# Performance work log

Hardware: AMD Instinct MI355X
Metric: run time of the kernel (lower is better)

The kernel has to match this reference:

```python
import jax, jax.numpy as jnp
import numpy as np

N_FFT = 64
HOP = 32
PAD = N_FFT // 2

def _window():
    # torch.hann_window(n_fft) is periodic: 0.5*(1 - cos(2*pi*n/N))
    n = jnp.arange(N_FFT, dtype=jnp.float32)
    return 0.5 * (1.0 - jnp.cos(2.0 * jnp.pi * n / N_FFT))

def _frame_idx(n_frames):
    return jnp.arange(n_frames)[:, None] * HOP + jnp.arange(N_FFT)[None, :]

def _stft(x):
    # x: [..., T] -> complex spectrogram [..., n_frames, F] (torch center=True, reflect pad)
    xp = jnp.pad(x, [(0, 0)] * (x.ndim - 1) + [(PAD, PAD)], mode='reflect')
    Tp = xp.shape[-1]
    n_frames = (Tp - N_FFT) // HOP + 1
    frames = xp[..., _frame_idx(n_frames)] * _window()  # [..., n_frames, n_fft]
    return jnp.fft.rfft(frames, axis=-1)

def _istft(spec, T):
    # spec: [..., n_frames, F] -> signal [..., T] (torch istft with length=T)
    w = _window()
    frames = jnp.fft.irfft(spec, n=N_FFT, axis=-1) * w  # [..., n_frames, n_fft]
    n_frames = frames.shape[-2]
    Tp = T + 2 * PAD
    idx = _frame_idx(n_frames)
    ola = jnp.zeros(frames.shape[:-2] + (Tp,), frames.dtype).at[..., idx].add(frames)
    env = jnp.zeros((Tp,), frames.dtype).at[idx].add(w * w)
    env = jnp.where(env > 1e-11, env, 1.0)
    return (ola / env)[..., PAD:PAD + T]

def reference(x, weight):
    # x: [B, C_in, T], weight: [C_out, C_in, F]
    B, C, T = x.shape
    U = _stft(x)  # [B, C_in, n_frames, F] complex
    # Linearity: sum over input channels in frequency domain, then one ISTFT per output channel.
    Yr = jnp.einsum('oif,binf->bonf', weight, U.real)
    Yi = jnp.einsum('oif,binf->bonf', weight, U.imag)
    Y = Yr + 1j * Yi  # [B, C_out, n_frames, F]
    return _istft(Y, T)  # [B, C_out, T]

def setup_inputs() -> dict:
    key = jax.random.key(0)
    k1, k2 = jax.random.split(key)
    B, C_in, C_out, T = 8, 64, 64, 16384
    x = jax.random.normal(k1, (B, C_in, T), dtype=jnp.float32)
    weight = jax.random.normal(k2, (C_out, C_in, N_FFT // 2 + 1), dtype=jnp.float32)
    return {"x": x, "weight": weight}
```

## Files before the change

kernel.cpp:

```cpp
#include <hip/hip_runtime.h>
#include <cstddef>

#define TT 16384
#define NFRAMES 513
#define NFP 520
#define BNP (8 * NFP)
#define PI32 0.09817477042468103870f

typedef unsigned int u32;
typedef unsigned short u16;
typedef __attribute__((ext_vector_type(8))) short bf16x8;
typedef __attribute__((ext_vector_type(4))) float f32x4;

#define TAB_WBF 0
#define TAB_BM  (33 * 64 * 72)
#define TAB_BTA (TAB_BM + 80 * 72)
#define TAB_TOT (TAB_BTA + 64 * 72)
#define TF_EINV 0

__device__ __forceinline__ float b2f(u16 h) {
  union { u32 u; float f; } v; v.u = ((u32)h) << 16; return v.f;
}
__device__ __forceinline__ u16 f2b(float f) {
  union { float f; u32 u; } v; v.f = f;
  const u32 r = v.u + 0x7FFFu + ((v.u >> 16) & 1u);
  return (u16)(r >> 16);
}
__device__ __forceinline__ u32 pack2(float a, float b) {
  return (u32)f2b(a) | ((u32)f2b(b) << 16);
}

__global__ __launch_bounds__(256) void k0_tables(const float* __restrict__ W,
                                                 u16* __restrict__ t16,
                                                 float* __restrict__ tf) {
  const int b = blockIdx.x, tid = threadIdx.x;
  if (b < 33) {
    for (int idx = tid; idx < 64 * 72; idx += 256) {
      const int o = idx / 72, i = idx % 72;
      const float v = (i < 64) ? W[(size_t)(o * 64 + i) * 33 + b] : 0.f;
      t16[TAB_WBF + b * 64 * 72 + idx] = f2b(v);
    }
  } else if (b == 33) {
    for (int idx = tid; idx < 80 * 72; idx += 256) {
      const int fc = idx / 72, j = idx % 72;
      float v = 0.f;
      if (j < 64 && fc < 65) {
        const float wj = 0.5f * (1.0f - cosf((float)j * PI32));
        if (fc < 64) {
          const int f = fc >> 1;
          const float ang = (float)((f * j) & 63) * PI32;
          v = wj * ((fc & 1) ? -sinf(ang) : cosf(ang));
        } else {
          v = (j & 1) ? -wj : wj;
        }
      }
      t16[TAB_BM + idx] = f2b(v);
    }
  } else {
    for (int idx = tid; idx < 64 * 72; idx += 256) {
      const int j = idx / 72, cf = idx % 72;
      float v = 0.f;
      if (cf < 65) {
        const int f = cf >> 1;
        const float wj = 0.5f * (1.0f - cosf((float)j * PI32));
        const float sc = ((f == 0) || (f == 32)) ? 0.015625f : 0.03125f;
        const float ang = (float)((f * j) & 63) * PI32;
        v = wj * sc * ((cf & 1) ? -sinf(ang) : cosf(ang));
      }
      t16[TAB_BTA + idx] = f2b(v);
    }
    if (tid < 32) {
      const float c = cosf((float)tid * PI32);
      tf[TF_EINV + tid] = 2.0f / (1.0f + c * c);
    }
  }
}

__global__ __launch_bounds__(256) void k1_stft(const float* __restrict__ x,
                                               const u16* __restrict__ t16,
                                               u16* __restrict__ U) {
  const int tile = blockIdx.x;
  const int ch   = blockIdx.y;
  const int b    = blockIdx.z;
  const int tid = threadIdx.x;
  __shared__ __align__(16) u16 Bm[80 * 72];
  __shared__ __align__(16) u16 Awt[64 * 72];
  __shared__ __align__(16) u16 Cs[66 * 72];
  __shared__ float xef[64];

  for (int k = tid; k < 720; k += 256)
    ((uint4*)Bm)[k] = ((const uint4*)(t16 + TAB_BM))[k];

  const float* xb = x + (size_t)(b * 64 + ch) * TT;

  if (tile == 8) {
    if (tid < 64) {
      const int t = (tid < 32) ? (16352 + tid) : (16414 - tid);
      xef[tid] = xb[t];
    }
    __syncthreads();
    if (tid < 66) {
      float s = 0.f;
#pragma unroll 8
      for (int j = 0; j < 64; ++j)
        s = fmaf(xef[j], b2f(Bm[tid * 72 + j]), s);
      U[(size_t)(tid * 64 + ch) * BNP + b * NFP + 512] = f2b(s);
    }
    return;
  }

  const int F0 = tile * 64;
  if (tile == 0) {
    if (tid < 32) Awt[tid] = f2b(xb[32 - tid]);
    for (int c = 8 + tid; c < 520; c += 256) {
      const float4 v = *(const float4*)(xb + 4 * c - 32);
      const uint2 pk = make_uint2(pack2(v.x, v.y), pack2(v.z, v.w));
      const int flb = c >> 3, jj = 4 * (c & 7);
      if (flb < 64) *(uint2*)&Awt[flb * 72 + jj] = pk;
      *(uint2*)&Awt[(flb - 1) * 72 + 32 + jj] = pk;
    }
  } else {
    const float* src = xb + 32 * F0 - 32;
    for (int c = tid; c < 520; c += 256) {
      const float4 v = *(const float4*)(src + 4 * c);
      const uint2 pk = make_uint2(pack2(v.x, v.y), pack2(v.z, v.w));
      const int flb = c >> 3, jj = 4 * (c & 7);
      if (flb < 64) *(uint2*)&Awt[flb * 72 + jj] = pk;
      if (flb >= 1) *(uint2*)&Awt[(flb - 1) * 72 + 32 + jj] = pk;
    }
  }
  __syncthreads();

  const int wave = tid >> 6, lane = tid & 63;
  const int n = lane & 15, quad = lane >> 4;

  bf16x8 bfr[4][2];
#pragma unroll
  for (int nt = 0; nt < 4; ++nt)
#pragma unroll
    for (int ks = 0; ks < 2; ++ks)
      bfr[nt][ks] = *(const bf16x8*)&Awt[(nt * 16 + n) * 72 + ks * 32 + quad * 8];

  const int npass = (wave == 0) ? 2 : 1;
  for (int pass = 0; pass < npass; ++pass) {
    const int mt = pass ? 4 : wave;
    bf16x8 af[2];
#pragma unroll
    for (int ks = 0; ks < 2; ++ks)
      af[ks] = *(const bf16x8*)&Bm[(mt * 16 + n) * 72 + ks * 32 + quad * 8];
    f32x4 acc[4];
#pragma unroll
    for (int nt = 0; nt < 4; ++nt) acc[nt] = (f32x4){0.f, 0.f, 0.f, 0.f};
#pragma unroll
    for (int ks = 0; ks < 2; ++ks)
#pragma unroll
      for (int nt = 0; nt < 4; ++nt)
        acc[nt] = __builtin_amdgcn_mfma_f32_16x16x32_bf16(af[ks], bfr[nt][ks],
                                                          acc[nt], 0, 0, 0);
#pragma unroll
    for (int nt = 0; nt < 4; ++nt) {
      const int fl = nt * 16 + n;
#pragma unroll
      for (int r = 0; r < 4; ++r) {
        const int fc = mt * 16 + quad * 4 + r;
        if (fc < 66) Cs[fc * 72 + fl] = f2b(acc[nt][r]);
      }
    }
  }
  __syncthreads();

  const int bnb = b * NFP + F0;
  for (int k = tid; k < 528; k += 256) {
    const int fc = k >> 3, part = k & 7;
    *(uint4*)(U + (size_t)(fc * 64 + ch) * BNP + bnb + part * 8) =
        *(const uint4*)&Cs[fc * 72 + part * 8];
  }
}

__global__ __launch_bounds__(256) void k2_mix(const u16* __restrict__ t16,
                                              u16* __restrict__ U) {
  const int f   = blockIdx.y;
  const int bn0 = blockIdx.x * 64;
  const int tid = threadIdx.x;
  __shared__ __align__(16) u16 Ut[2 * 64 * 72];
  __shared__ __align__(16) u16 Wl[64 * 72];

  for (int k = tid; k < 576; k += 256)
    ((uint4*)Wl)[k] = ((const uint4*)(t16 + TAB_WBF + f * 64 * 72))[k];

#pragma unroll
  for (int kk = 0; kk < 4; ++kk) {
    const int id = tid + kk * 256;
    const int c = id >> 9, rem = id & 511;
    const int i = rem >> 3, qc = rem & 7;
    const uint4 raw = *(const uint4*)(U + (size_t)((2 * f + c) * 64 + i) * BNP + bn0 + 8 * qc);
    const int col = (((i >> 3) ^ qc) << 3) + (i & 7);
    u16* base = &Ut[c * 4608 + col];
#pragma unroll
    for (int e = 0; e < 8; ++e) {
      const u32 w = ((const u32*)&raw)[e >> 1];
      base[(8 * qc + e) * 72] = (u16)((e & 1) ? (w >> 16) : (w & 0xFFFFu));
    }
  }
  __syncthreads();

  const int wave = tid >> 6, lane = tid & 63;
  const int n = lane & 15, quad = lane >> 4;
  const int mt = wave;

  bf16x8 af[2];
#pragma unroll
  for (int ks = 0; ks < 2; ++ks)
    af[ks] = *(const bf16x8*)&Wl[(mt * 16 + n) * 72 + ks * 32 + quad * 8];

  f32x4 acc[4][2];
#pragma unroll
  for (int nt = 0; nt < 4; ++nt)
#pragma unroll
    for (int c = 0; c < 2; ++c) acc[nt][c] = (f32x4){0.f, 0.f, 0.f, 0.f};

#pragma unroll
  for (int ks = 0; ks < 2; ++ks)
#pragma unroll
    for (int nt = 0; nt < 4; ++nt) {
      const int q = nt * 16 + n;
      const int chunk = (((ks << 2) + quad) ^ ((q >> 3) & 7)) << 3;
#pragma unroll
      for (int c = 0; c < 2; ++c) {
        const bf16x8 bf = *(const bf16x8*)&Ut[c * 4608 + q * 72 + chunk];
        acc[nt][c] = __builtin_amdgcn_mfma_f32_16x16x32_bf16(af[ks], bf,
                                                             acc[nt][c], 0, 0, 0);
      }
    }
  __syncthreads();

#pragma unroll
  for (int nt = 0; nt < 4; ++nt) {
    const int col = nt * 16 + n;
#pragma unroll
    for (int c = 0; c < 2; ++c)
#pragma unroll
      for (int r = 0; r < 4; ++r) {
        const int o = mt * 16 + quad * 4 + r;
        Ut[(c * 64 + o) * 72 + col] = f2b(acc[nt][c][r]);
      }
  }
  __syncthreads();

  for (int k = tid; k < 1024; k += 256) {
    const int row = k >> 3, part = k & 7;
    const int c = row >> 6, o = row & 63;
    *(uint4*)(U + (size_t)((2 * f + c) * 64 + o) * BNP + bn0 + part * 8) =
        *(const uint4*)&Ut[row * 72 + part * 8];
  }
}

__global__ __launch_bounds__(256) void k3_istft(const u16* __restrict__ Y,
                                                const u16* __restrict__ t16,
                                                const float* __restrict__ tf,
                                                float* __restrict__ out) {
  const int tile = blockIdx.x;
  const int o    = blockIdx.y;
  const int b    = blockIdx.z;
  const int n0 = tile * 64;
  const int tid = threadIdx.x;
  __shared__ __align__(16) u16 BtA[64 * 72];
  __shared__ __align__(16) u16 Yt[80 * 64];
  __shared__ __align__(16) u16 y64[72];
  __shared__ float Csh[65 * 68];
  __shared__ float einv[32];

  for (int k = tid; k < 576; k += 256)
    ((uint4*)BtA)[k] = ((const uint4*)(t16 + TAB_BTA))[k];

  const size_t ybase = (size_t)b * NFP + n0;
  for (int id = tid; id < 576; id += 256) {
    const int cf = id / 9, oct = id % 9;
    const uint4 raw = *(const uint4*)(Y + (size_t)(cf * 64 + o) * BNP + ybase + oct * 8);
    const u16* s = (const u16*)&raw;
#pragma unroll
    for (int e = 0; e < 8; ++e) {
      const int row = oct * 8 + e;
      const int sw = (row ^ (row >> 3)) & 7;
      Yt[row * 64 + ((((cf >> 3) ^ sw) << 3) | (cf & 7))] = s[e];
    }
  }
  if (tid < 9)
    *(uint4*)&y64[tid * 8] =
        *(const uint4*)(Y + (size_t)(64 * 64 + o) * BNP + ybase + tid * 8);
  if (tid < 32) einv[tid] = tf[TF_EINV + tid];
  __syncthreads();

  const int wave = tid >> 6, lane = tid & 63;
  const int n = lane & 15, quad = lane >> 4;
  const int mt = wave;

  bf16x8 af[2];
#pragma unroll
  for (int ks = 0; ks < 2; ++ks)
    af[ks] = *(const bf16x8*)&BtA[(mt * 16 + n) * 72 + ks * 32 + quad * 8];

  float a64v[4];
#pragma unroll
  for (int r = 0; r < 4; ++r)
    a64v[r] = b2f(BtA[(mt * 16 + quad * 4 + r) * 72 + 64]);

  f32x4 acc[5];
#pragma unroll
  for (int nt = 0; nt < 5; ++nt) acc[nt] = (f32x4){0.f, 0.f, 0.f, 0.f};
#pragma unroll
  for (int nt = 0; nt < 5; ++nt) {
    const int row = nt * 16 + n;
    const int sw = (row ^ (row >> 3)) & 7;
    const u16* yrow = &Yt[row * 64];
#pragma unroll
    for (int ks = 0; ks < 2; ++ks) {
      const bf16x8 bf = *(const bf16x8*)&yrow[((ks * 4 + quad) ^ sw) << 3];
      acc[nt] = __builtin_amdgcn_mfma_f32_16x16x32_bf16(af[ks], bf, acc[nt], 0, 0, 0);
    }
  }
#pragma unroll
  for (int nt = 0; nt < 5; ++nt) {
    const int fl = nt * 16 + n;
    if (nt < 4 || n == 0) {
      const float yv = b2f(y64[fl]);
      *(float4*)&Csh[fl * 68 + mt * 16 + quad * 4] =
          make_float4(fmaf(yv, a64v[0], acc[nt][0]),
                      fmaf(yv, a64v[1], acc[nt][1]),
                      fmaf(yv, a64v[2], acc[nt][2]),
                      fmaf(yv, a64v[3], acc[nt][3]));
    }
  }
  __syncthreads();

  const int q0 = 8 * tid;
  const int j2 = q0 & 31;
  const int fl2 = 1 + (q0 >> 5);
  const float4 lo0 = *(const float4*)&Csh[fl2 * 68 + j2];
  const float4 lo1 = *(const float4*)&Csh[fl2 * 68 + j2 + 4];
  const float4 hi0 = *(const float4*)&Csh[(fl2 - 1) * 68 + j2 + 32];
  const float4 hi1 = *(const float4*)&Csh[(fl2 - 1) * 68 + j2 + 36];
  float v[8] = {lo0.x + hi0.x, lo0.y + hi0.y, lo0.z + hi0.z, lo0.w + hi0.w,
                lo1.x + hi1.x, lo1.y + hi1.y, lo1.z + hi1.z, lo1.w + hi1.w};
#pragma unroll
  for (int k = 0; k < 8; ++k) v[k] *= einv[j2 + k];
  float* po = out + (size_t)(b * 64 + o) * TT + 32 * n0 + q0;
  *(float4*)po       = make_float4(v[0], v[1], v[2], v[3]);
  *(float4*)(po + 4) = make_float4(v[4], v[5], v[6], v[7]);
}

extern "C" void kernel_launch(void* const* d_in, const int* in_sizes, int n_in,
                              void* d_out, int out_size, void* d_ws, size_t ws_size,
                              hipStream_t stream) {
  const float* x  = (const float*)d_in[0];
  const float* wt = (const float*)d_in[1];
  float* out = (float*)d_out;
  u16* U = (u16*)d_ws;
  u16* t16 = (u16*)((char*)d_ws + (size_t)66 * 64 * BNP * 2);
  float* tf = (float*)(t16 + TAB_TOT);

  dim3 blk(256);
  k0_tables<<<dim3(35),       blk, 0, stream>>>(wt, t16, tf);
  k1_stft  <<<dim3(9, 64, 8), blk, 0, stream>>>(x, t16, U);
  k2_mix   <<<dim3(65, 33),   blk, 0, stream>>>(t16, U);
  k3_istft <<<dim3(8, 64, 8), blk, 0, stream>>>(U, t16, tf, out);
}
```

Before: 139.8 us.

## Process two channels per block in STFT/ISTFT and fold weight table into STFT launch

STFT and ISTFT blocks now each handle two channels, so the constant basis tables loaded into shared memory are reused across two channels and the grid shrinks by half. The bf16 weight-table transpose moves out of k0_tables into extra blocks of the k1_stft launch (tile index 9), shrinking k0 to two blocks and overlapping the weight conversion with STFT work. The trade-off is more shared memory per block, fewer blocks for latency hiding, and an extra barrier inside the ISTFT loop.

```diff
diff --git a/kernel.cpp b/kernel.cpp
--- a/kernel.cpp
+++ b/kernel.cpp
@@ -30,17 +30,10 @@
   return (u32)f2b(a) | ((u32)f2b(b) << 16);
 }
 
-__global__ __launch_bounds__(256) void k0_tables(const float* __restrict__ W,
-                                                 u16* __restrict__ t16,
+__global__ __launch_bounds__(256) void k0_tables(u16* __restrict__ t16,
                                                  float* __restrict__ tf) {
   const int b = blockIdx.x, tid = threadIdx.x;
-  if (b < 33) {
-    for (int idx = tid; idx < 64 * 72; idx += 256) {
-      const int o = idx / 72, i = idx % 72;
-      const float v = (i < 64) ? W[(size_t)(o * 64 + i) * 33 + b] : 0.f;
-      t16[TAB_WBF + b * 64 * 72 + idx] = f2b(v);
-    }
-  } else if (b == 33) {
+  if (b == 0) {
     for (int idx = tid; idx < 80 * 72; idx += 256) {
       const int fc = idx / 72, j = idx % 72;
       float v = 0.f;
@@ -77,56 +70,74 @@
 }
 
 __global__ __launch_bounds__(256) void k1_stft(const float* __restrict__ x,
-                                               const u16* __restrict__ t16,
+                                               const float* __restrict__ W,
+                                               u16* __restrict__ t16,
                                                u16* __restrict__ U) {
   const int tile = blockIdx.x;
-  const int ch   = blockIdx.y;
+  const int ch0  = blockIdx.y * 2;
   const int b    = blockIdx.z;
   const int tid = threadIdx.x;
+
+  if (tile == 9) {
+    const int flat = blockIdx.y * 8 + b;
+    for (int idx = flat * 256 + tid; idx < 33 * 64 * 72; idx += 256 * 256) {
+      const int f = idx / 4608, rem = idx % 4608;
+      const int o = rem / 72, i = rem % 72;
+      const float v = (i < 64) ? W[(size_t)(o * 64 + i) * 33 + f] : 0.f;
+      t16[TAB_WBF + idx] = f2b(v);
+    }
+    return;
+  }
+
   __shared__ __align__(16) u16 Bm[80 * 72];
-  __shared__ __align__(16) u16 Awt[64 * 72];
-  __shared__ __align__(16) u16 Cs[66 * 72];
-  __shared__ float xef[64];
+  __shared__ __align__(16) u16 Awt[2 * 64 * 72];
+  __shared__ __align__(16) u16 Cs2[66 * 152];
+  __shared__ float xef[2][64];
 
   for (int k = tid; k < 720; k += 256)
     ((uint4*)Bm)[k] = ((const uint4*)(t16 + TAB_BM))[k];
 
-  const float* xb = x + (size_t)(b * 64 + ch) * TT;
-
   if (tile == 8) {
-    if (tid < 64) {
-      const int t = (tid < 32) ? (16352 + tid) : (16414 - tid);
-      xef[tid] = xb[t];
+    if (tid < 128) {
+      const int c = tid >> 6, j = tid & 63;
+      const int t = (j < 32) ? (16352 + j) : (16414 - j);
+      xef[c][j] = x[(size_t)(b * 64 + ch0 + c) * TT + t];
     }
     __syncthreads();
-    if (tid < 66) {
+    for (int id = tid; id < 132; id += 256) {
+      const int c = id / 66, fc = id % 66;
       float s = 0.f;
 #pragma unroll 8
       for (int j = 0; j < 64; ++j)
-        s = fmaf(xef[j], b2f(Bm[tid * 72 + j]), s);
-      U[(size_t)(tid * 64 + ch) * BNP + b * NFP + 512] = f2b(s);
+        s = fmaf(xef[c][j], b2f(Bm[fc * 72 + j]), s);
+      U[(size_t)(fc * 64 + ch0 + c) * BNP + b * NFP + 512] = f2b(s);
     }
     return;
   }
 
   const int F0 = tile * 64;
-  if (tile == 0) {
-    if (tid < 32) Awt[tid] = f2b(xb[32 - tid]);
-    for (int c = 8 + tid; c < 520; c += 256) {
-      const float4 v = *(const float4*)(xb + 4 * c - 32);
-      const uint2 pk = make_uint2(pack2(v.x, v.y), pack2(v.z, v.w));
-      const int flb = c >> 3, jj = 4 * (c & 7);
-      if (flb < 64) *(uint2*)&Awt[flb * 72 + jj] = pk;
-      *(uint2*)&Awt[(flb - 1) * 72 + 32 + jj] = pk;
-    }
-  } else {
-    const float* src = xb + 32 * F0 - 32;
-    for (int c = tid; c < 520; c += 256) {
-      const float4 v = *(const float4*)(src + 4 * c);
-      const uint2 pk = make_uint2(pack2(v.x, v.y), pack2(v.z, v.w));
-      const int flb = c >> 3, jj = 4 * (c & 7);
-      if (flb < 64) *(uint2*)&Awt[flb * 72 + jj] = pk;
-      if (flb >= 1) *(uint2*)&Awt[(flb - 1) * 72 + 32 + jj] = pk;
+#pragma unroll
+  for (int cc = 0; cc < 2; ++cc) {
+    const float* xb = x + (size_t)(b * 64 + ch0 + cc) * TT;
+    u16* Aw = &Awt[cc * 4608];
+    if (tile == 0) {
+      if (tid < 32) Aw[tid] = f2b(xb[32 - tid]);
+      for (int c = 8 + tid; c < 520; c += 256) {
+        const float4 v = *(const float4*)(xb + 4 * c - 32);
+        const uint2 pk = make_uint2(pack2(v.x, v.y), pack2(v.z, v.w));
+        const int flb = c >> 3, jj = 4 * (c & 7);
+        if (flb < 64) *(uint2*)&Aw[flb * 72 + jj] = pk;
+        *(uint2*)&Aw[(flb - 1) * 72 + 32 + jj] = pk;
+      }
+    } else {
+      const float* src = xb + 32 * F0 - 32;
+      for (int c = tid; c < 520; c += 256) {
+        const float4 v = *(const float4*)(src + 4 * c);
+        const uint2 pk = make_uint2(pack2(v.x, v.y), pack2(v.z, v.w));
+        const int flb = c >> 3, jj = 4 * (c & 7);
+        if (flb < 64) *(uint2*)&Aw[flb * 72 + jj] = pk;
+        if (flb >= 1) *(uint2*)&Aw[(flb - 1) * 72 + 32 + jj] = pk;
+      }
     }
   }
   __syncthreads();
@@ -134,46 +145,72 @@
   const int wave = tid >> 6, lane = tid & 63;
   const int n = lane & 15, quad = lane >> 4;
 
-  bf16x8 bfr[4][2];
-#pragma unroll
-  for (int nt = 0; nt < 4; ++nt)
+  bf16x8 afm[2], afx[2];
+#pragma unroll
+  for (int ks = 0; ks < 2; ++ks)
+    afm[ks] = *(const bf16x8*)&Bm[(wave * 16 + n) * 72 + ks * 32 + quad * 8];
+  if (wave == 0) {
 #pragma unroll
     for (int ks = 0; ks < 2; ++ks)
-      bfr[nt][ks] = *(const bf16x8*)&Awt[(nt * 16 + n) * 72 + ks * 32 + quad * 8];
-
-  const int npass = (wave == 0) ? 2 : 1;
-  for (int pass = 0; pass < npass; ++pass) {
-    const int mt = pass ? 4 : wave;
-    bf16x8 af[2];
+      afx[ks] = *(const bf16x8*)&Bm[(64 + n) * 72 + ks * 32 + quad * 8];
+  }
+
+  for (int cc = 0; cc < 2; ++cc) {
+    bf16x8 bfr[4][2];
+#pragma unroll
+    for (int nt = 0; nt < 4; ++nt)
+#pragma unroll
+      for (int ks = 0; ks < 2; ++ks)
+        bfr[nt][ks] =
+            *(const bf16x8*)&Awt[cc * 4608 + (nt * 16 + n) * 72 + ks * 32 + quad * 8];
+
+    f32x4 acc[4];
+#pragma unroll
+    for (int nt = 0; nt < 4; ++nt) acc[nt] = (f32x4){0.f, 0.f, 0.f, 0.f};
 #pragma unroll
     for (int ks = 0; ks < 2; ++ks)
-      af[ks] = *(const bf16x8*)&Bm[(mt * 16 + n) * 72 + ks * 32 + quad * 8];
-    f32x4 acc[4];
-#pragma unroll
-    for (int nt = 0; nt < 4; ++nt) acc[nt] = (f32x4){0.f, 0.f, 0.f, 0.f};
-#pragma unroll
-    for (int ks = 0; ks < 2; ++ks)
 #pragma unroll
       for (int nt = 0; nt < 4; ++nt)
-        acc[nt] = __builtin_amdgcn_mfma_f32_16x16x32_bf16(af[ks], bfr[nt][ks],
+        acc[nt] = __builtin_amdgcn_mfma_f32_16x16x32_bf16(afm[ks], bfr[nt][ks],
                                                           acc[nt], 0, 0, 0);
 #pragma unroll
     for (int nt = 0; nt < 4; ++nt) {
       const int fl = nt * 16 + n;
 #pragma unroll
       for (int r = 0; r < 4; ++r) {
-        const int fc = mt * 16 + quad * 4 + r;
-        if (fc < 66) Cs[fc * 72 + fl] = f2b(acc[nt][r]);
+        const int fc = wave * 16 + quad * 4 + r;
+        Cs2[fc * 152 + cc * 72 + fl] = f2b(acc[nt][r]);
+      }
+    }
+
+    if (wave == 0) {
+      f32x4 acx[4];
+#pragma unroll
+      for (int nt = 0; nt < 4; ++nt) acx[nt] = (f32x4){0.f, 0.f, 0.f, 0.f};
+#pragma unroll
+      for (int ks = 0; ks < 2; ++ks)
+#pragma unroll
+        for (int nt = 0; nt < 4; ++nt)
+          acx[nt] = __builtin_amdgcn_mfma_f32_16x16x32_bf16(afx[ks], bfr[nt][ks],
+                                                            acx[nt], 0, 0, 0);
+#pragma unroll
+      for (int nt = 0; nt < 4; ++nt) {
+        const int fl = nt * 16 + n;
+#pragma unroll
+        for (int r = 0; r < 4; ++r) {
+          const int fc = 64 + quad * 4 + r;
+          if (fc < 66) Cs2[fc * 152 + cc * 72 + fl] = f2b(acx[nt][r]);
+        }
       }
     }
   }
   __syncthreads();
 
   const int bnb = b * NFP + F0;
-  for (int k = tid; k < 528; k += 256) {
-    const int fc = k >> 3, part = k & 7;
-    *(uint4*)(U + (size_t)(fc * 64 + ch) * BNP + bnb + part * 8) =
-        *(const uint4*)&Cs[fc * 72 + part * 8];
+  for (int k = tid; k < 1056; k += 256) {
+    const int fc = k >> 4, c = (k >> 3) & 1, part = k & 7;
+    *(uint4*)(U + (size_t)(fc * 64 + ch0 + c) * BNP + bnb + part * 8) =
+        *(const uint4*)&Cs2[fc * 152 + c * 72 + part * 8];
   }
 }
 
@@ -260,13 +297,13 @@
                                                 const float* __restrict__ tf,
                                                 float* __restrict__ out) {
   const int tile = blockIdx.x;
-  const int o    = blockIdx.y;
+  const int o0   = blockIdx.y * 2;
   const int b    = blockIdx.z;
   const int n0 = tile * 64;
   const int tid = threadIdx.x;
   __shared__ __align__(16) u16 BtA[64 * 72];
-  __shared__ __align__(16) u16 Yt[80 * 64];
-  __shared__ __align__(16) u16 y64[72];
+  __shared__ __align__(16) u16 Yt[2][80 * 64];
+  __shared__ __align__(16) u16 y64[2][72];
   __shared__ float Csh[65 * 68];
   __shared__ float einv[32];
 
@@ -274,20 +311,23 @@
     ((uint4*)BtA)[k] = ((const uint4*)(t16 + TAB_BTA))[k];
 
   const size_t ybase = (size_t)b * NFP + n0;
-  for (int id = tid; id < 576; id += 256) {
-    const int cf = id / 9, oct = id % 9;
-    const uint4 raw = *(const uint4*)(Y + (size_t)(cf * 64 + o) * BNP + ybase + oct * 8);
+  for (int id = tid; id < 1152; id += 256) {
+    const int oo = id / 576, rid = id % 576;
+    const int cf = rid / 9, oct = rid % 9;
+    const uint4 raw = *(const uint4*)(Y + (size_t)(cf * 64 + o0 + oo) * BNP + ybase + oct * 8);
     const u16* s = (const u16*)&raw;
 #pragma unroll
     for (int e = 0; e < 8; ++e) {
       const int row = oct * 8 + e;
       const int sw = (row ^ (row >> 3)) & 7;
-      Yt[row * 64 + ((((cf >> 3) ^ sw) << 3) | (cf & 7))] = s[e];
-    }
-  }
-  if (tid < 9)
-    *(uint4*)&y64[tid * 8] =
-        *(const uint4*)(Y + (size_t)(64 * 64 + o) * BNP + ybase + tid * 8);
+      Yt[oo][row * 64 + ((((cf >> 3) ^ sw) << 3) | (cf & 7))] = s[e];
+    }
+  }
+  if (tid < 18) {
+    const int oo = tid / 9, part = tid % 9;
+    *(uint4*)&y64[oo][part * 8] =
+        *(const uint4*)(Y + (size_t)(64 * 64 + o0 + oo) * BNP + ybase + part * 8);
+  }
   if (tid < 32) einv[tid] = tf[TF_EINV + tid];
   __syncthreads();
 
@@ -305,48 +345,51 @@
   for (int r = 0; r < 4; ++r)
     a64v[r] = b2f(BtA[(mt * 16 + quad * 4 + r) * 72 + 64]);
 
-  f32x4 acc[5];
-#pragma unroll
-  for (int nt = 0; nt < 5; ++nt) acc[nt] = (f32x4){0.f, 0.f, 0.f, 0.f};
-#pragma unroll
-  for (int nt = 0; nt < 5; ++nt) {
-    const int row = nt * 16 + n;
-    const int sw = (row ^ (row >> 3)) & 7;
-    const u16* yrow = &Yt[row * 64];
-#pragma unroll
-    for (int ks = 0; ks < 2; ++ks) {
-      const bf16x8 bf = *(const bf16x8*)&yrow[((ks * 4 + quad) ^ sw) << 3];
-      acc[nt] = __builtin_amdgcn_mfma_f32_16x16x32_bf16(af[ks], bf, acc[nt], 0, 0, 0);
-    }
-  }
-#pragma unroll
-  for (int nt = 0; nt < 5; ++nt) {
-    const int fl = nt * 16 + n;
-    if (nt < 4 || n == 0) {
-      const float yv = b2f(y64[fl]);
-      *(float4*)&Csh[fl * 68 + mt * 16 + quad * 4] =
-          make_float4(fmaf(yv, a64v[0], acc[nt][0]),
-                      fmaf(yv, a64v[1], acc[nt][1]),
-                      fmaf(yv, a64v[2], acc[nt][2]),
-                      fmaf(yv, a64v[3], acc[nt][3]));
-    }
-  }
-  __syncthreads();
-
-  const int q0 = 8 * tid;
-  const int j2 = q0 & 31;
-  const int fl2 = 1 + (q0 >> 5);
-  const float4 lo0 = *(const float4*)&Csh[fl2 * 68 + j2];
-  const float4 lo1 = *(const float4*)&Csh[fl2 * 68 + j2 + 4];
-  const float4 hi0 = *(const float4*)&Csh[(fl2 - 1) * 68 + j2 + 32];
-  const float4 hi1 = *(const float4*)&Csh[(fl2 - 1) * 68 + j2 + 36];
-  float v[8] = {lo0.x + hi0.x, lo0.y + hi0.y, lo0.z + hi0.z, lo0.w + hi0.w,
-                lo1.x + hi1.x, lo1.y + hi1.y, lo1.z + hi1.z, lo1.w + hi1.w};
-#pragma unroll
-  for (int k = 0; k < 8; ++k) v[k] *= einv[j2 + k];
-  float* po = out + (size_t)(b * 64 + o) * TT + 32 * n0 + q0;
-  *(float4*)po       = make_float4(v[0], v[1], v[2], v[3]);
-  *(float4*)(po + 4) = make_float4(v[4], v[5], v[6], v[7]);
+  for (int oo = 0; oo < 2; ++oo) {
+    f32x4 acc[5];
+#pragma unroll
+    for (int nt = 0; nt < 5; ++nt) acc[nt] = (f32x4){0.f, 0.f, 0.f, 0.f};
+#pragma unroll
+    for (int nt = 0; nt < 5; ++nt) {
+      const int row = nt * 16 + n;
+      const int sw = (row ^ (row >> 3)) & 7;
+      const u16* yrow = &Yt[oo][row * 64];
+#pragma unroll
+      for (int ks = 0; ks < 2; ++ks) {
+        const bf16x8 bf = *(const bf16x8*)&yrow[((ks * 4 + quad) ^ sw) << 3];
+        acc[nt] = __builtin_amdgcn_mfma_f32_16x16x32_bf16(af[ks], bf, acc[nt], 0, 0, 0);
+      }
+    }
+#pragma unroll
+    for (int nt = 0; nt < 5; ++nt) {
+      const int fl = nt * 16 + n;
+      if (nt < 4 || n == 0) {
+        const float yv = b2f(y64[oo][fl]);
+        *(float4*)&Csh[fl * 68 + mt * 16 + quad * 4] =
+            make_float4(fmaf(yv, a64v[0], acc[nt][0]),
+                        fmaf(yv, a64v[1], acc[nt][1]),
+                        fmaf(yv, a64v[2], acc[nt][2]),
+                        fmaf(yv, a64v[3], acc[nt][3]));
+      }
+    }
+    __syncthreads();
+
+    const int q0 = 8 * tid;
+    const int j2 = q0 & 31;
+    const int fl2 = 1 + (q0 >> 5);
+    const float4 lo0 = *(const float4*)&Csh[fl2 * 68 + j2];
+    const float4 lo1 = *(const float4*)&Csh[fl2 * 68 + j2 + 4];
+    const float4 hi0 = *(const float4*)&Csh[(fl2 - 1) * 68 + j2 + 32];
+    const float4 hi1 = *(const float4*)&Csh[(fl2 - 1) * 68 + j2 + 36];
+    float v[8] = {lo0.x + hi0.x, lo0.y + hi0.y, lo0.z + hi0.z, lo0.w + hi0.w,
+                  lo1.x + hi1.x, lo1.y + hi1.y, lo1.z + hi1.z, lo1.w + hi1.w};
+#pragma unroll
+    for (int k = 0; k < 8; ++k) v[k] *= einv[j2 + k];
+    float* po = out + (size_t)(b * 64 + o0 + oo) * TT + 32 * n0 + q0;
+    *(float4*)po       = make_float4(v[0], v[1], v[2], v[3]);
+    *(float4*)(po + 4) = make_float4(v[4], v[5], v[6], v[7]);
+    if (oo == 0) __syncthreads();
+  }
 }
 
 extern "C" void kernel_launch(void* const* d_in, const int* in_sizes, int n_in,
@@ -360,8 +403,8 @@
   float* tf = (float*)(t16 + TAB_TOT);
 
   dim3 blk(256);
-  k0_tables<<<dim3(35),       blk, 0, stream>>>(wt, t16, tf);
-  k1_stft  <<<dim3(9, 64, 8), blk, 0, stream>>>(x, t16, U);
+  k0_tables<<<dim3(2),        blk, 0, stream>>>(t16, tf);
+  k1_stft  <<<dim3(10, 32, 8), blk, 0, stream>>>(x, wt, t16, U);
   k2_mix   <<<dim3(65, 33),   blk, 0, stream>>>(t16, U);
-  k3_istft <<<dim3(8, 64, 8), blk, 0, stream>>>(U, t16, tf, out);
-}
+  k3_istft <<<dim3(8, 32, 8), blk, 0, stream>>>(U, t16, tf, out);
+}
```

Measured after the change: 142.7 us. 2.1% more time.

## Do iSTFT overlap-add in registers via ds_bpermute instead of LDS staging

Applied to the files above, without the earlier changes.

Permutes the rows of the synthesis basis fed to the MFMA so that each wave holds both halves of the overlapping frame samples. The overlap-add between adjacent frames then uses cross-lane ds_bpermute rather than a 17 KB shared-memory tile and an extra barrier. Removing the Csh buffer cuts LDS per block and adds a launch-bounds occupancy hint of 6. In exchange, half the lanes (quad>=2) sit idle during the stores, and the stores become narrower and more scattered.

```diff
diff --git a/kernel.cpp b/kernel.cpp
--- a/kernel.cpp
+++ b/kernel.cpp
@@ -255,10 +255,10 @@
   }
 }
 
-__global__ __launch_bounds__(256) void k3_istft(const u16* __restrict__ Y,
-                                                const u16* __restrict__ t16,
-                                                const float* __restrict__ tf,
-                                                float* __restrict__ out) {
+__global__ __launch_bounds__(256, 6) void k3_istft(const u16* __restrict__ Y,
+                                                   const u16* __restrict__ t16,
+                                                   const float* __restrict__ tf,
+                                                   float* __restrict__ out) {
   const int tile = blockIdx.x;
   const int o    = blockIdx.y;
   const int b    = blockIdx.z;
@@ -267,8 +267,7 @@
   __shared__ __align__(16) u16 BtA[64 * 72];
   __shared__ __align__(16) u16 Yt[80 * 64];
   __shared__ __align__(16) u16 y64[72];
-  __shared__ float Csh[65 * 68];
-  __shared__ float einv[32];
+  __shared__ __align__(16) float einv[32];
 
   for (int k = tid; k < 576; k += 256)
     ((uint4*)BtA)[k] = ((const uint4*)(t16 + TAB_BTA))[k];
@@ -293,17 +292,20 @@
 
   const int wave = tid >> 6, lane = tid & 63;
   const int n = lane & 15, quad = lane >> 4;
-  const int mt = wave;
-
+
+  const int jrowA = wave * 8 + (n & 7) + (n >> 3) * 32;
   bf16x8 af[2];
 #pragma unroll
   for (int ks = 0; ks < 2; ++ks)
-    af[ks] = *(const bf16x8*)&BtA[(mt * 16 + n) * 72 + ks * 32 + quad * 8];
+    af[ks] = *(const bf16x8*)&BtA[jrowA * 72 + ks * 32 + quad * 8];
 
   float a64v[4];
 #pragma unroll
-  for (int r = 0; r < 4; ++r)
-    a64v[r] = b2f(BtA[(mt * 16 + quad * 4 + r) * 72 + 64]);
+  for (int r = 0; r < 4; ++r) {
+    const int c = quad * 4 + r;
+    const int j = wave * 8 + (c & 7) + (c >> 3) * 32;
+    a64v[r] = b2f(BtA[j * 72 + 64]);
+  }
 
   f32x4 acc[5];
 #pragma unroll
@@ -319,34 +321,37 @@
       acc[nt] = __builtin_amdgcn_mfma_f32_16x16x32_bf16(af[ks], bf, acc[nt], 0, 0, 0);
     }
   }
+
+  const int srcl = (((n + 15) & 15) | ((2 | (quad & 1)) << 4)) << 2;
+  const float4 ev = *(const float4*)&einv[wave * 8 + (quad & 1) * 4];
+  float* pob = out + (size_t)(b * 64 + o) * TT + 32 * n0 + wave * 8 + (quad & 1) * 4;
+  float hiPrev[4] = {0.f, 0.f, 0.f, 0.f};
 #pragma unroll
   for (int nt = 0; nt < 5; ++nt) {
     const int fl = nt * 16 + n;
     if (nt < 4 || n == 0) {
       const float yv = b2f(y64[fl]);
-      *(float4*)&Csh[fl * 68 + mt * 16 + quad * 4] =
-          make_float4(fmaf(yv, a64v[0], acc[nt][0]),
-                      fmaf(yv, a64v[1], acc[nt][1]),
-                      fmaf(yv, a64v[2], acc[nt][2]),
-                      fmaf(yv, a64v[3], acc[nt][3]));
-    }
-  }
-  __syncthreads();
-
-  const int q0 = 8 * tid;
-  const int j2 = q0 & 31;
-  const int fl2 = 1 + (q0 >> 5);
-  const float4 lo0 = *(const float4*)&Csh[fl2 * 68 + j2];
-  const float4 lo1 = *(const float4*)&Csh[fl2 * 68 + j2 + 4];
-  const float4 hi0 = *(const float4*)&Csh[(fl2 - 1) * 68 + j2 + 32];
-  const float4 hi1 = *(const float4*)&Csh[(fl2 - 1) * 68 + j2 + 36];
-  float v[8] = {lo0.x + hi0.x, lo0.y + hi0.y, lo0.z + hi0.z, lo0.w + hi0.w,
-                lo1.x + hi1.x, lo1.y + hi1.y, lo1.z + hi1.z, lo1.w + hi1.w};
-#pragma unroll
-  for (int k = 0; k < 8; ++k) v[k] *= einv[j2 + k];
-  float* po = out + (size_t)(b * 64 + o) * TT + 32 * n0 + q0;
-  *(float4*)po       = make_float4(v[0], v[1], v[2], v[3]);
-  *(float4*)(po + 4) = make_float4(v[4], v[5], v[6], v[7]);
+#pragma unroll
+      for (int r = 0; r < 4; ++r) acc[nt][r] = fmaf(yv, a64v[r], acc[nt][r]);
+    }
+    float cur[4];
+#pragma unroll
+    for (int r = 0; r < 4; ++r)
+      cur[r] = __int_as_float(
+          __builtin_amdgcn_ds_bpermute(srcl, __float_as_int(acc[nt][r])));
+    if (quad < 2) {
+      const bool valid = (nt < 4) ? (fl > 0) : (n == 0);
+      if (valid) {
+        float v[4];
+#pragma unroll
+        for (int r = 0; r < 4; ++r)
+          v[r] = (acc[nt][r] + ((n == 0) ? hiPrev[r] : cur[r])) * ev[r];
+        *(float4*)(pob + (fl - 1) * 32) = make_float4(v[0], v[1], v[2], v[3]);
+      }
+    }
+#pragma unroll
+    for (int r = 0; r < 4; ++r) hiPrev[r] = cur[r];
+  }
 }
 
 extern "C" void kernel_launch(void* const* d_in, const int* in_sizes, int n_in,
```

Result: no change. 139.8 us (+0.0%).
